# Optimization experiments

Hardware: AMD Instinct MI355X
Metric: run time of the kernel (lower is better)

Reference implementation:

```python
import jax, jax.numpy as jnp
import numpy as np

DIM = 768
HEAD = 12
DK = DIM // HEAD

def setup_inputs() -> dict:
    key = jax.random.key(0)
    ks = jax.random.split(key, 9)
    B, L = 4, 2048
    s = 1.0 / np.sqrt(DIM)
    qkv = jax.random.normal(ks[0], (B, L, DIM), dtype=jnp.float32)
    mask = jnp.ones((B, L), dtype=jnp.int32)
    Wq = jax.random.normal(ks[1], (DIM, DIM), dtype=jnp.float32) * s
    bq = jnp.zeros((DIM,), dtype=jnp.float32)
    Wk = jax.random.normal(ks[2], (DIM, DIM), dtype=jnp.float32) * s
    bk = jnp.zeros((DIM,), dtype=jnp.float32)
    Wv = jax.random.normal(ks[3], (DIM, DIM), dtype=jnp.float32) * s
    bv = jnp.zeros((DIM,), dtype=jnp.float32)
    Wo = jax.random.normal(ks[4], (DIM, DIM), dtype=jnp.float32) * s
    bo = jnp.zeros((DIM,), dtype=jnp.float32)
    return {"qkv": qkv, "mask": mask, "Wq": Wq, "bq": bq, "Wk": Wk, "bk": bk,
            "Wv": Wv, "bv": bv, "Wo": Wo, "bo": bo}

def reference(qkv, mask, Wq, bq, Wk, bk, Wv, bv, Wo, bo):
    B, L, _ = qkv.shape
    def proj(W, b):
        # [B,L,dim] -> [B,H,L,dk]
        return (qkv @ W + b).reshape(B, L, HEAD, DK).transpose(0, 2, 1, 3)
    q, k, v = proj(Wq, bq), proj(Wk, bk), proj(Wv, bv)
    scores = jnp.einsum('bhqd,bhkd->bhqk', q, k) / jnp.sqrt(jnp.float32(DK))
    # mask: [B,L] broadcast over heads and query positions (key axis)
    m = mask[:, None, None, :]  # [B,1,1,L]
    scores = jnp.where(m == 0, jnp.float32(-1e9), scores)
    p = jax.nn.softmax(scores, axis=-1)
    x = jnp.einsum('bhqk,bhkd->bhqd', p, v)  # [B,H,L,dk]
    x = x.transpose(0, 2, 1, 3).reshape(B, L, DIM)
    return x @ Wo + bo
```

## Files before the change

### kernel.cpp

```cpp
#include <hip/hip_runtime.h>
#include <hip/hip_bf16.h>
#include <stdint.h>

#define DIM  768
#define NHEAD 12
#define DK   64
#define BATCH 4
#define SEQ  2048
#define ROWS (BATCH*SEQ)
#define SCL  0.1803368801111204f

typedef __bf16 bf16_t;
typedef bf16_t bf16x8 __attribute__((ext_vector_type(8)));
typedef bf16_t bf16x4 __attribute__((ext_vector_type(4)));
typedef float  f32x4  __attribute__((ext_vector_type(4)));
typedef float  f32x16 __attribute__((ext_vector_type(16)));

typedef unsigned int __attribute__((address_space(1)))* as1p;
typedef unsigned int __attribute__((address_space(3)))* as3p;

__device__ __forceinline__ void gload_lds16(const void* g, void* l) {
    __builtin_amdgcn_global_load_lds((as1p)g, (as3p)l, 16, 0, 0);
}
#define MEMFENCE asm volatile("" ::: "memory")

__global__ void cast_bf16_kernel(const float* __restrict__ in, bf16_t* __restrict__ out) {
    int i = blockIdx.x * 256 + threadIdx.x;
    const float4* p = (const float4*)in;
    float4 a = p[(size_t)i*2], b = p[(size_t)i*2+1];
    bf16x8 v;
    v[0]=(bf16_t)a.x; v[1]=(bf16_t)a.y; v[2]=(bf16_t)a.z; v[3]=(bf16_t)a.w;
    v[4]=(bf16_t)b.x; v[5]=(bf16_t)b.y; v[6]=(bf16_t)b.z; v[7]=(bf16_t)b.w;
    *(bf16x8*)(out + (size_t)i*8) = v;
}

__global__ void wtrans_kernel(const float* __restrict__ W0, const float* __restrict__ W1,
                              const float* __restrict__ W2, const float* __restrict__ W3,
                              bf16_t* __restrict__ T0, bf16_t* __restrict__ T1,
                              bf16_t* __restrict__ T2, bf16_t* __restrict__ T3) {
    const float* W = blockIdx.z==0?W0 : blockIdx.z==1?W1 : blockIdx.z==2?W2 : W3;
    bf16_t*      T = blockIdx.z==0?T0 : blockIdx.z==1?T1 : blockIdx.z==2?T2 : T3;
    __shared__ float tile[32][33];
    int tx = threadIdx.x, ty = threadIdx.y;
    int c = blockIdx.x*32 + tx;
    #pragma unroll
    for (int r = 0; r < 32; r += 8)
        tile[ty+r][tx] = W[(size_t)(blockIdx.y*32 + ty + r)*DIM + c];
    __syncthreads();
    int oc = blockIdx.y*32 + tx;
    #pragma unroll
    for (int r = 0; r < 32; r += 8)
        T[(size_t)(blockIdx.x*32 + ty + r)*DIM + oc] = (bf16_t)tile[tx][ty+r];
}

template<int MODE>
__global__ __launch_bounds__(256) void gemm_kernel(
    const bf16_t* __restrict__ A,
    const bf16_t* __restrict__ WTa, const bf16_t* __restrict__ WTb, const bf16_t* __restrict__ WTc,
    const float* __restrict__ ba, const float* __restrict__ bb, const float* __restrict__ bc,
    bf16_t* __restrict__ Qo, bf16_t* __restrict__ Ko, bf16_t* __restrict__ Vo,
    float* __restrict__ Oo) {
    __shared__ __align__(16) bf16_t As[2][128*32];
    __shared__ __align__(16) bf16_t Bs[2][128*32];
    const int tid = threadIdx.x, wave = tid>>6, lane = tid&63;
    const int wm = wave>>1, wn = wave&1;
    const int b = blockIdx.x;
    const int xcd = b & 7, ib = b >> 3;
    int z, ntile, mtile;
    if (MODE == 0) { z = ib % 3; ntile = (ib/3) % 6; mtile = xcd*8 + ib/18; }
    else           { z = 0;      ntile = ib % 6;     mtile = xcd*8 + ib/6;  }
    const int m0 = mtile*128, n0 = ntile*128;
    const bf16_t* WT  = (z==0) ? WTa : (z==1 ? WTb : WTc);
    const float* bias = (z==0) ? ba  : (z==1 ? bb  : bc);

    f32x4 acc[4][4];
    const f32x4 zf = {0.f,0.f,0.f,0.f};
    #pragma unroll
    for (int m = 0; m < 4; ++m)
        #pragma unroll
        for (int n = 0; n < 4; ++n) acc[m][n] = zf;

    const int srow = wave*32 + (lane>>2);
    const int scol = (lane&3)*8;
    const bf16_t* Ag = A  + (size_t)(m0+srow)*DIM + scol;
    const bf16_t* Bg = WT + (size_t)(n0+srow)*DIM + scol;

    #pragma unroll
    for (int i2 = 0; i2 < 2; ++i2) {
        gload_lds16(Ag + (size_t)(i2*16)*DIM, &As[0][(wave*32 + i2*16)*32]);
        gload_lds16(Bg + (size_t)(i2*16)*DIM, &Bs[0][(wave*32 + i2*16)*32]);
    }

    int cur = 0;
    for (int t = 0; t < DIM/32; ++t) {
        if (t < DIM/32 - 1) {
            const size_t k1 = (size_t)(t+1)*32;
            #pragma unroll
            for (int i2 = 0; i2 < 2; ++i2) {
                gload_lds16(Ag + (size_t)(i2*16)*DIM + k1, &As[cur^1][(wave*32 + i2*16)*32]);
                gload_lds16(Bg + (size_t)(i2*16)*DIM + k1, &Bs[cur^1][(wave*32 + i2*16)*32]);
            }
            asm volatile("s_waitcnt vmcnt(4)" ::: "memory");
        } else {
            asm volatile("s_waitcnt vmcnt(0)" ::: "memory");
        }
        MEMFENCE; __builtin_amdgcn_s_barrier(); MEMFENCE;

        bf16x8 af[4], bfr[4];
        #pragma unroll
        for (int m = 0; m < 4; ++m)
            af[m]  = *(const bf16x8*)&As[cur][(wm*64 + m*16 + (lane&15))*32 + (lane>>4)*8];
        #pragma unroll
        for (int n = 0; n < 4; ++n)
            bfr[n] = *(const bf16x8*)&Bs[cur][(wn*64 + n*16 + (lane&15))*32 + (lane>>4)*8];
        #pragma unroll
        for (int m = 0; m < 4; ++m)
            #pragma unroll
            for (int n = 0; n < 4; ++n)
                acc[m][n] = __builtin_amdgcn_mfma_f32_16x16x32_bf16(af[m], bfr[n], acc[m][n], 0, 0, 0);

        MEMFENCE; __builtin_amdgcn_s_barrier(); MEMFENCE;
        cur ^= 1;
    }

    float bvv[4];
    #pragma unroll
    for (int n = 0; n < 4; ++n) bvv[n] = bias[n0 + wn*64 + n*16 + (lane&15)];

    #pragma unroll
    for (int m = 0; m < 4; ++m) {
        #pragma unroll
        for (int n = 0; n < 4; ++n) {
            #pragma unroll
            for (int r = 0; r < 4; ++r) {
                float val = acc[m][n][r] + bvv[n];
                int R = m0 + wm*64 + m*16 + (lane>>4)*4 + r;
                int C = n0 + wn*64 + n*16 + (lane&15);
                if (MODE == 1) {
                    Oo[(size_t)R*DIM + C] = val;
                } else {
                    int bi = R>>11, li = R&2047, h = C>>6, d = C&63;
                    size_t bh = (size_t)(bi*NHEAD + h);
                    if      (z==0) Qo[(bh*SEQ + li)*DK + d] = (bf16_t)(val*SCL);
                    else if (z==1) Ko[(bh*SEQ + li)*DK + d] = (bf16_t)val;
                    else {
                        int li2 = (li & ~12) | ((li&4)<<1) | ((li&8)>>1);
                        Vo[(bh*DK + d)*SEQ + li2] = (bf16_t)val;
                    }
                }
            }
        }
    }
}

#define NT (SEQ/64)

__global__ __launch_bounds__(256) void attn_kernel(
    const bf16_t* __restrict__ Q, const bf16_t* __restrict__ K, const bf16_t* __restrict__ VT,
    const int* __restrict__ mask, bf16_t* __restrict__ X) {
    __shared__ __align__(16) bf16_t lds[2*8192];
    const int tid = threadIdx.x, wv = tid>>6, lane = tid&63;
    const int lo5 = lane&31, hi5 = lane>>5;
    const int b = blockIdx.x;
    const int xcd = b & 7, ii = b >> 3;
    const int bh = xcd*6 + (ii>>4), qt = ii & 15;
    const int bi = bh/NHEAD, h = bh%NHEAD;
    const bf16_t* Qb = Q  + (size_t)bh*SEQ*DK;
    const bf16_t* Kb = K  + (size_t)bh*SEQ*DK;
    const bf16_t* Vb = VT + (size_t)bh*DK*SEQ;
    const int* mk = mask + (size_t)bi*SEQ + lo5;
    const int q0 = qt*128 + wv*32;

    int mOk = 1;
    {
        const int4* m4 = (const int4*)(mask + (size_t)bi*SEQ);
        #pragma unroll
        for (int i2 = 0; i2 < 8; ++i2) {
            int4 v = m4[lane + i2*64];
            mOk &= (v.x != 0) & (v.y != 0) & (v.z != 0) & (v.w != 0);
        }
    }
    const int mAll = __all(mOk);

    bf16x8 qf[4];
    #pragma unroll
    for (int ks = 0; ks < 4; ++ks)
        qf[ks] = *(const bf16x8*)&Qb[(size_t)(q0 + lo5)*DK + ks*16 + hi5*8];

    f32x16 O0, O1;
    #pragma unroll
    for (int r = 0; r < 16; ++r) { O0[r] = 0.f; O1[r] = 0.f; }
    float lsum = 0.f;

    bf16x8 onesb = {};
    if (hi5 == 0) onesb[0] = (bf16_t)1.0f;

    const int srow  = wv*16 + (lane>>3);
    const int sslot = (lane&7) ^ (srow&7);
    const bf16_t* Kg = Kb + (size_t)srow*DK  + sslot*8;
    const bf16_t* Vg = Vb + (size_t)srow*SEQ + sslot*8;
    int koff[4];
    #pragma unroll
    for (int ks = 0; ks < 4; ++ks) koff[ks] = (((2*ks + hi5) ^ (lo5 & 7)) << 3);

    #pragma unroll
    for (int i = 0; i < 2; ++i) {
        gload_lds16(Kg + (size_t)(i*8)*DK,  lds +        (wv*16 + i*8)*64);
        gload_lds16(Vg + (size_t)(i*8)*SEQ, lds + 4096 + (wv*16 + i*8)*64);
    }

    int cur = 0;
    for (int t = 0; t < NT; ++t) {
        const int kv0 = t*64;
        if (t < NT-1) {
            bf16_t* nb = lds + (cur^1)*8192;
            #pragma unroll
            for (int i = 0; i < 2; ++i) {
                gload_lds16(Kg + (size_t)(kv0+64)*DK + (size_t)(i*8)*DK,  nb +        (wv*16 + i*8)*64);
                gload_lds16(Vg + (kv0+64)            + (size_t)(i*8)*SEQ, nb + 4096 + (wv*16 + i*8)*64);
            }
            asm volatile("s_waitcnt vmcnt(4)" ::: "memory");
        } else {
            asm volatile("s_waitcnt vmcnt(0)" ::: "memory");
        }
        MEMFENCE; __builtin_amdgcn_s_barrier(); MEMFENCE;

        const bf16_t* Kt = lds + cur*8192;
        const bf16_t* Vt = lds + cur*8192 + 4096;

        f32x16 s0, s1;
        #pragma unroll
        for (int r = 0; r < 16; ++r) { s0[r] = -12.f; s1[r] = -12.f; }
        #pragma unroll
        for (int ks = 0; ks < 4; ++ks) {
            bf16x8 a0 = *(const bf16x8*)&Kt[ lo5     *64 + koff[ks]];
            bf16x8 a1 = *(const bf16x8*)&Kt[(32+lo5)*64 + koff[ks]];
            s0 = __builtin_amdgcn_mfma_f32_32x32x16_bf16(a0, qf[ks], s0, 0, 0, 0);
            s1 = __builtin_amdgcn_mfma_f32_32x32x16_bf16(a1, qf[ks], s1, 0, 0, 0);
        }
        if (!mAll) {
            int mv0 = mk[kv0], mv1 = mk[kv0 + 32];
            bf16x8 ba = {};
            ba[0] = mv0 ? (bf16_t)0.f : (bf16_t)(-1024.0f);
            s0 = __builtin_amdgcn_mfma_f32_32x32x16_bf16(ba, onesb, s0, 0, 0, 0);
            ba[0] = mv1 ? (bf16_t)0.f : (bf16_t)(-1024.0f);
            s1 = __builtin_amdgcn_mfma_f32_32x32x16_bf16(ba, onesb, s1, 0, 0, 0);
        }

        #pragma unroll
        for (int r = 0; r < 16; ++r) {
            s0[r] = __builtin_amdgcn_exp2f(s0[r]);
            s1[r] = __builtin_amdgcn_exp2f(s1[r]);
        }
        float t01[16];
        #pragma unroll
        for (int r = 0; r < 16; ++r) t01[r] = s0[r] + s1[r];
        float u[8];
        #pragma unroll
        for (int r = 0; r < 8; ++r) u[r] = t01[r] + t01[r+8];
        float w0 = (u[0]+u[1]) + (u[2]+u[3]);
        float w1 = (u[4]+u[5]) + (u[6]+u[7]);
        float ps = w0 + w1;
        lsum += ps + __shfl_xor(ps, 32);

        bf16x8 pf0, pf1, pf2, pf3;
        #pragma unroll
        for (int j = 0; j < 8; ++j) {
            pf0[j] = (bf16_t)s0[j];
            pf1[j] = (bf16_t)s0[8+j];
            pf2[j] = (bf16_t)s1[j];
            pf3[j] = (bf16_t)s1[8+j];
        }

        #pragma unroll
        for (int ks = 0; ks < 4; ++ks) {
            bf16x8 pb = (ks==0) ? pf0 : (ks==1) ? pf1 : (ks==2) ? pf2 : pf3;
            bf16x8 a0 = *(const bf16x8*)&Vt[ lo5     *64 + koff[ks]];
            bf16x8 a1 = *(const bf16x8*)&Vt[(32+lo5)*64 + koff[ks]];
            O0 = __builtin_amdgcn_mfma_f32_32x32x16_bf16(a0, pb, O0, 0, 0, 0);
            O1 = __builtin_amdgcn_mfma_f32_32x32x16_bf16(a1, pb, O1, 0, 0, 0);
        }
        MEMFENCE; __builtin_amdgcn_s_barrier(); MEMFENCE;
        cur ^= 1;
    }

    float rl = __builtin_amdgcn_rcpf(lsum);
    const size_t rowb = (size_t)(bi*SEQ + q0 + lo5)*DIM + h*DK;
    #pragma unroll
    for (int g = 0; g < 4; ++g) {
        bf16x4 v0, v1;
        #pragma unroll
        for (int j = 0; j < 4; ++j) {
            v0[j] = (bf16_t)(O0[g*4+j] * rl);
            v1[j] = (bf16_t)(O1[g*4+j] * rl);
        }
        *(bf16x4*)&X[rowb + g*8 + hi5*4]      = v0;
        *(bf16x4*)&X[rowb + 32 + g*8 + hi5*4] = v1;
    }
}

extern "C" void kernel_launch(void* const* d_in, const int* in_sizes, int n_in,
                              void* d_out, int out_size, void* d_ws, size_t ws_size,
                              hipStream_t stream) {
    (void)in_sizes; (void)n_in; (void)out_size; (void)ws_size;
    const float* qkv = (const float*)d_in[0];
    const int*  mask = (const int*)d_in[1];
    const float* Wq = (const float*)d_in[2];
    const float* bq = (const float*)d_in[3];
    const float* Wk = (const float*)d_in[4];
    const float* bk = (const float*)d_in[5];
    const float* Wv = (const float*)d_in[6];
    const float* bv = (const float*)d_in[7];
    const float* Wo = (const float*)d_in[8];
    const float* bo = (const float*)d_in[9];
    float* out = (float*)d_out;

    char* ws = (char*)d_ws;
    size_t off = 0;
    auto carve = [&](size_t bytes) { void* p = ws + off; off += (bytes + 255) & ~(size_t)255; return p; };
    const size_t actN = (size_t)ROWS*DIM;
    bf16_t* Abf = (bf16_t*)carve(actN*2);
    bf16_t* WTq = (bf16_t*)carve((size_t)DIM*DIM*2);
    bf16_t* WTk = (bf16_t*)carve((size_t)DIM*DIM*2);
    bf16_t* WTv = (bf16_t*)carve((size_t)DIM*DIM*2);
    bf16_t* WTo = (bf16_t*)carve((size_t)DIM*DIM*2);
    bf16_t* Qb  = (bf16_t*)carve(actN*2);
    bf16_t* Kb  = (bf16_t*)carve(actN*2);
    bf16_t* VTb = (bf16_t*)carve(actN*2);
    bf16_t* Xb  = (bf16_t*)carve(actN*2);

    cast_bf16_kernel<<<dim3(ROWS*DIM/8/256), dim3(256), 0, stream>>>(qkv, Abf);
    wtrans_kernel<<<dim3(24,24,4), dim3(32,8), 0, stream>>>(Wq, Wk, Wv, Wo, WTq, WTk, WTv, WTo);
    gemm_kernel<0><<<dim3(1152), dim3(256), 0, stream>>>(Abf, WTq, WTk, WTv, bq, bk, bv,
                                                         Qb, Kb, VTb, nullptr);
    attn_kernel<<<dim3(768), dim3(256), 0, stream>>>(Qb, Kb, VTb, mask, Xb);
    gemm_kernel<1><<<dim3(384), dim3(256), 0, stream>>>(Xb, WTo, WTo, WTo, bo, bo, bo,
                                                        nullptr, nullptr, nullptr, out);
}
```

Before: 173.2 us.

## Enlarge GEMM tiles to 256x128 with 8 waves and triple-buffered LDS pipeline

The projection GEMMs now use 512-thread blocks, each computing a 256x128 output tile with 8 waves arranged 4x2, which halves the grid size. Global-to-LDS loads switch from double to triple buffering with a two-stage prefetch distance, and the vmcnt waits are adjusted to match. The aim is to hide more memory latency and reuse each B tile across more rows. In exchange, LDS use per block grows to about 72KB and there are fewer blocks (192 for the output projection, below the CU count), which may hurt occupancy and load balance.

```diff
diff --git a/kernel.cpp b/kernel.cpp
--- a/kernel.cpp
+++ b/kernel.cpp
@@ -54,22 +54,22 @@
 }
 
 template<int MODE>
-__global__ __launch_bounds__(256) void gemm_kernel(
+__global__ __launch_bounds__(512) void gemm_kernel(
     const bf16_t* __restrict__ A,
     const bf16_t* __restrict__ WTa, const bf16_t* __restrict__ WTb, const bf16_t* __restrict__ WTc,
     const float* __restrict__ ba, const float* __restrict__ bb, const float* __restrict__ bc,
     bf16_t* __restrict__ Qo, bf16_t* __restrict__ Ko, bf16_t* __restrict__ Vo,
     float* __restrict__ Oo) {
-    __shared__ __align__(16) bf16_t As[2][128*32];
-    __shared__ __align__(16) bf16_t Bs[2][128*32];
+    __shared__ __align__(16) bf16_t As[3][256*32];
+    __shared__ __align__(16) bf16_t Bs[3][128*32];
     const int tid = threadIdx.x, wave = tid>>6, lane = tid&63;
     const int wm = wave>>1, wn = wave&1;
     const int b = blockIdx.x;
     const int xcd = b & 7, ib = b >> 3;
     int z, ntile, mtile;
-    if (MODE == 0) { z = ib % 3; ntile = (ib/3) % 6; mtile = xcd*8 + ib/18; }
-    else           { z = 0;      ntile = ib % 6;     mtile = xcd*8 + ib/6;  }
-    const int m0 = mtile*128, n0 = ntile*128;
+    if (MODE == 0) { z = ib % 3; ntile = (ib/3) % 6; mtile = xcd*4 + ib/18; }
+    else           { z = 0;      ntile = ib % 6;     mtile = xcd*4 + ib/6;  }
+    const int m0 = mtile*256, n0 = ntile*128;
     const bf16_t* WT  = (z==0) ? WTa : (z==1 ? WTb : WTc);
     const float* bias = (z==0) ? ba  : (z==1 ? bb  : bc);
 
@@ -80,27 +80,30 @@
         #pragma unroll
         for (int n = 0; n < 4; ++n) acc[m][n] = zf;
 
-    const int srow = wave*32 + (lane>>2);
+    const int srow = wave*16 + (lane>>2);
     const int scol = (lane&3)*8;
     const bf16_t* Ag = A  + (size_t)(m0+srow)*DIM + scol;
     const bf16_t* Bg = WT + (size_t)(n0+srow)*DIM + scol;
-
-    #pragma unroll
-    for (int i2 = 0; i2 < 2; ++i2) {
-        gload_lds16(Ag + (size_t)(i2*16)*DIM, &As[0][(wave*32 + i2*16)*32]);
-        gload_lds16(Bg + (size_t)(i2*16)*DIM, &Bs[0][(wave*32 + i2*16)*32]);
-    }
-
+    const int aoff0 = (wave*16)*32, aoff1 = (128 + wave*16)*32, boff = (wave*16)*32;
+
+    #define GEMM_STAGE(BUF, KOFF)                                              \
+        gload_lds16(Ag + (KOFF),                     &As[BUF][aoff0]);         \
+        gload_lds16(Ag + (size_t)128*DIM + (KOFF),   &As[BUF][aoff1]);         \
+        gload_lds16(Bg + (KOFF),                     &Bs[BUF][boff]);
+
+    GEMM_STAGE(0, 0)
+    GEMM_STAGE(1, 32)
+
+    const int NTK = DIM/32;
     int cur = 0;
-    for (int t = 0; t < DIM/32; ++t) {
-        if (t < DIM/32 - 1) {
-            const size_t k1 = (size_t)(t+1)*32;
-            #pragma unroll
-            for (int i2 = 0; i2 < 2; ++i2) {
-                gload_lds16(Ag + (size_t)(i2*16)*DIM + k1, &As[cur^1][(wave*32 + i2*16)*32]);
-                gload_lds16(Bg + (size_t)(i2*16)*DIM + k1, &Bs[cur^1][(wave*32 + i2*16)*32]);
-            }
-            asm volatile("s_waitcnt vmcnt(4)" ::: "memory");
+    for (int t = 0; t < NTK; ++t) {
+        if (t + 2 < NTK) {
+            int b2 = cur + 2; if (b2 >= 3) b2 -= 3;
+            const size_t k2 = (size_t)(t+2)*32;
+            GEMM_STAGE(b2, k2)
+            asm volatile("s_waitcnt vmcnt(6)" ::: "memory");
+        } else if (t + 1 < NTK) {
+            asm volatile("s_waitcnt vmcnt(3)" ::: "memory");
         } else {
             asm volatile("s_waitcnt vmcnt(0)" ::: "memory");
         }
@@ -120,8 +123,9 @@
                 acc[m][n] = __builtin_amdgcn_mfma_f32_16x16x32_bf16(af[m], bfr[n], acc[m][n], 0, 0, 0);
 
         MEMFENCE; __builtin_amdgcn_s_barrier(); MEMFENCE;
-        cur ^= 1;
-    }
+        cur = (cur == 2) ? 0 : cur + 1;
+    }
+    #undef GEMM_STAGE
 
     float bvv[4];
     #pragma unroll
@@ -331,9 +335,9 @@
 
     cast_bf16_kernel<<<dim3(ROWS*DIM/8/256), dim3(256), 0, stream>>>(qkv, Abf);
     wtrans_kernel<<<dim3(24,24,4), dim3(32,8), 0, stream>>>(Wq, Wk, Wv, Wo, WTq, WTk, WTv, WTo);
-    gemm_kernel<0><<<dim3(1152), dim3(256), 0, stream>>>(Abf, WTq, WTk, WTv, bq, bk, bv,
-                                                         Qb, Kb, VTb, nullptr);
+    gemm_kernel<0><<<dim3(576), dim3(512), 0, stream>>>(Abf, WTq, WTk, WTv, bq, bk, bv,
+                                                        Qb, Kb, VTb, nullptr);
     attn_kernel<<<dim3(768), dim3(256), 0, stream>>>(Qb, Kb, VTb, mask, Xb);
-    gemm_kernel<1><<<dim3(384), dim3(256), 0, stream>>>(Xb, WTo, WTo, WTo, bo, bo, bo,
+    gemm_kernel<1><<<dim3(192), dim3(512), 0, stream>>>(Xb, WTo, WTo, WTo, bo, bo, bo,
                                                         nullptr, nullptr, nullptr, out);
 }
```

After: 185.3 us. 7.0% more time.

## Use 256x256 tiles with 32x32x16 MFMA and swizzled LDS for QKV projection

Applied to the files above, without the earlier changes.

Splits the projection GEMM into a dedicated QKV kernel with 512 threads, 256x256 output tiles, K-step 64, XOR-swizzled LDS layout and 32x32x16 MFMA instructions, launched as 288 blocks instead of 1152. Larger tiles raise arithmetic intensity and cut redundant global loads, and the swizzle targets LDS bank conflicts. The output projection keeps the old 128x128 tiling in its own simplified kernel. In exchange the bigger tiles use much more LDS and registers per block, and 288 blocks may not fill all CUs well.

```diff
diff --git a/kernel.cpp b/kernel.cpp
--- a/kernel.cpp
+++ b/kernel.cpp
@@ -53,25 +53,117 @@
         T[(size_t)(blockIdx.x*32 + ty + r)*DIM + oc] = (bf16_t)tile[tx][ty+r];
 }
 
-template<int MODE>
-__global__ __launch_bounds__(256) void gemm_kernel(
+__global__ __launch_bounds__(512) void gemm0_kernel(
     const bf16_t* __restrict__ A,
-    const bf16_t* __restrict__ WTa, const bf16_t* __restrict__ WTb, const bf16_t* __restrict__ WTc,
-    const float* __restrict__ ba, const float* __restrict__ bb, const float* __restrict__ bc,
-    bf16_t* __restrict__ Qo, bf16_t* __restrict__ Ko, bf16_t* __restrict__ Vo,
-    float* __restrict__ Oo) {
+    const bf16_t* __restrict__ WTq, const bf16_t* __restrict__ WTk, const bf16_t* __restrict__ WTv,
+    const float* __restrict__ bq, const float* __restrict__ bk, const float* __restrict__ bv,
+    bf16_t* __restrict__ Qo, bf16_t* __restrict__ Ko, bf16_t* __restrict__ Vo) {
+    __shared__ __align__(16) bf16_t As[2][256*64];
+    __shared__ __align__(16) bf16_t Bs[2][256*64];
+    const int tid = threadIdx.x, wave = tid>>6, lane = tid&63;
+    const int lo5 = lane&31, hi5 = lane>>5;
+    const int wm = wave>>2, wn = wave&3;
+    const int b = blockIdx.x;
+    const int xcd = b & 7, ib = b >> 3;
+    const int mtile = xcd*4 + ib/9;
+    const int nn = ib % 9, z = nn/3, ntile = nn%3;
+    const int m0 = mtile*256, n0 = ntile*256;
+    const bf16_t* WT  = (z==0) ? WTq : (z==1 ? WTk : WTv);
+    const float* bias = (z==0) ? bq  : (z==1 ? bk  : bv);
+
+    f32x16 acc[4][2];
+    #pragma unroll
+    for (int m = 0; m < 4; ++m)
+        #pragma unroll
+        for (int n = 0; n < 2; ++n)
+            #pragma unroll
+            for (int r = 0; r < 16; ++r) acc[m][n][r] = 0.f;
+
+    const int srow  = wave*32 + (lane>>3);
+    const int sslot = (lane&7) ^ (srow&7);
+    const bf16_t* Ag = A  + (size_t)(m0+srow)*DIM + sslot*8;
+    const bf16_t* Bg = WT + (size_t)(n0+srow)*DIM + sslot*8;
+    int koff[4];
+    #pragma unroll
+    for (int ks = 0; ks < 4; ++ks) koff[ks] = (((2*ks + hi5) ^ (lo5 & 7)) << 3);
+
+    #define G0STAGE(BUF, K0)                                                     \
+        _Pragma("unroll")                                                        \
+        for (int i2 = 0; i2 < 4; ++i2) {                                         \
+            gload_lds16(Ag + (size_t)(i2*8)*DIM + (K0), &As[BUF][(wave*32 + i2*8)*64]); \
+            gload_lds16(Bg + (size_t)(i2*8)*DIM + (K0), &Bs[BUF][(wave*32 + i2*8)*64]); \
+        }
+
+    G0STAGE(0, 0)
+
+    int cur = 0;
+    const int NTK = DIM/64;
+    for (int t = 0; t < NTK; ++t) {
+        if (t < NTK-1) {
+            G0STAGE(cur^1, (size_t)(t+1)*64)
+            asm volatile("s_waitcnt vmcnt(8)" ::: "memory");
+        } else {
+            asm volatile("s_waitcnt vmcnt(0)" ::: "memory");
+        }
+        MEMFENCE; __builtin_amdgcn_s_barrier(); MEMFENCE;
+
+        #pragma unroll
+        for (int ks = 0; ks < 4; ++ks) {
+            bf16x8 af[4], bfr[2];
+            #pragma unroll
+            for (int m = 0; m < 4; ++m)
+                af[m]  = *(const bf16x8*)&As[cur][(wm*128 + m*32 + lo5)*64 + koff[ks]];
+            #pragma unroll
+            for (int n = 0; n < 2; ++n)
+                bfr[n] = *(const bf16x8*)&Bs[cur][(wn*64 + n*32 + lo5)*64 + koff[ks]];
+            #pragma unroll
+            for (int m = 0; m < 4; ++m)
+                #pragma unroll
+                for (int n = 0; n < 2; ++n)
+                    acc[m][n] = __builtin_amdgcn_mfma_f32_32x32x16_bf16(af[m], bfr[n], acc[m][n], 0, 0, 0);
+        }
+        MEMFENCE; __builtin_amdgcn_s_barrier(); MEMFENCE;
+        cur ^= 1;
+    }
+    #undef G0STAGE
+
+    float bv2[2];
+    #pragma unroll
+    for (int n = 0; n < 2; ++n) bv2[n] = bias[n0 + wn*64 + n*32 + lo5];
+
+    #pragma unroll
+    for (int m = 0; m < 4; ++m) {
+        #pragma unroll
+        for (int n = 0; n < 2; ++n) {
+            #pragma unroll
+            for (int r = 0; r < 16; ++r) {
+                float val = acc[m][n][r] + bv2[n];
+                int R = m0 + wm*128 + m*32 + (r&3) + 8*(r>>2) + 4*hi5;
+                int c = n0 + wn*64 + n*32 + lo5;
+                int bi = R>>11, li = R&2047, h = c>>6, d = c&63;
+                size_t bh = (size_t)(bi*NHEAD + h);
+                if      (z==0) Qo[(bh*SEQ + li)*DK + d] = (bf16_t)(val*SCL);
+                else if (z==1) Ko[(bh*SEQ + li)*DK + d] = (bf16_t)val;
+                else {
+                    int li2 = (li & ~12) | ((li&4)<<1) | ((li&8)>>1);
+                    Vo[(bh*DK + d)*SEQ + li2] = (bf16_t)val;
+                }
+            }
+        }
+    }
+}
+
+__global__ __launch_bounds__(256) void gemm1_kernel(
+    const bf16_t* __restrict__ A, const bf16_t* __restrict__ WT,
+    const float* __restrict__ bias, float* __restrict__ Oo) {
     __shared__ __align__(16) bf16_t As[2][128*32];
     __shared__ __align__(16) bf16_t Bs[2][128*32];
     const int tid = threadIdx.x, wave = tid>>6, lane = tid&63;
     const int wm = wave>>1, wn = wave&1;
     const int b = blockIdx.x;
     const int xcd = b & 7, ib = b >> 3;
-    int z, ntile, mtile;
-    if (MODE == 0) { z = ib % 3; ntile = (ib/3) % 6; mtile = xcd*8 + ib/18; }
-    else           { z = 0;      ntile = ib % 6;     mtile = xcd*8 + ib/6;  }
+    const int ntile = ib % 6, mtile = xcd*8 + ib/6;
     const int m0 = mtile*128, n0 = ntile*128;
-    const bf16_t* WT  = (z==0) ? WTa : (z==1 ? WTb : WTc);
-    const float* bias = (z==0) ? ba  : (z==1 ? bb  : bc);
 
     f32x4 acc[4][4];
     const f32x4 zf = {0.f,0.f,0.f,0.f};
@@ -133,21 +225,9 @@
         for (int n = 0; n < 4; ++n) {
             #pragma unroll
             for (int r = 0; r < 4; ++r) {
-                float val = acc[m][n][r] + bvv[n];
                 int R = m0 + wm*64 + m*16 + (lane>>4)*4 + r;
                 int C = n0 + wn*64 + n*16 + (lane&15);
-                if (MODE == 1) {
-                    Oo[(size_t)R*DIM + C] = val;
-                } else {
-                    int bi = R>>11, li = R&2047, h = C>>6, d = C&63;
-                    size_t bh = (size_t)(bi*NHEAD + h);
-                    if      (z==0) Qo[(bh*SEQ + li)*DK + d] = (bf16_t)(val*SCL);
-                    else if (z==1) Ko[(bh*SEQ + li)*DK + d] = (bf16_t)val;
-                    else {
-                        int li2 = (li & ~12) | ((li&4)<<1) | ((li&8)>>1);
-                        Vo[(bh*DK + d)*SEQ + li2] = (bf16_t)val;
-                    }
-                }
+                Oo[(size_t)R*DIM + C] = acc[m][n][r] + bvv[n];
             }
         }
     }
@@ -331,9 +411,8 @@
 
     cast_bf16_kernel<<<dim3(ROWS*DIM/8/256), dim3(256), 0, stream>>>(qkv, Abf);
     wtrans_kernel<<<dim3(24,24,4), dim3(32,8), 0, stream>>>(Wq, Wk, Wv, Wo, WTq, WTk, WTv, WTo);
-    gemm_kernel<0><<<dim3(1152), dim3(256), 0, stream>>>(Abf, WTq, WTk, WTv, bq, bk, bv,
-                                                         Qb, Kb, VTb, nullptr);
+    gemm0_kernel<<<dim3(288), dim3(512), 0, stream>>>(Abf, WTq, WTk, WTv, bq, bk, bv,
+                                                      Qb, Kb, VTb);
     attn_kernel<<<dim3(768), dim3(256), 0, stream>>>(Qb, Kb, VTb, mask, Xb);
-    gemm_kernel<1><<<dim3(384), dim3(256), 0, stream>>>(Xb, WTo, WTo, WTo, bo, bo, bo,
-                                                        nullptr, nullptr, nullptr, out);
-}
+    gemm1_kernel<<<dim3(384), dim3(256), 0, stream>>>(Xb, WTo, bo, out);
+}
```

After: 186.5 us. 7.6% more time.

## Load GEMM fragments directly from global memory, dropping LDS staging and barriers

Applied to the files above, without the earlier changes.

The projection GEMM kernel no longer stages A and W tiles through double-buffered shared memory with async global-to-LDS loads and barriers. Each wave now loads its MFMA operand fragments straight from global memory into registers, relying on the cache for reuse. The block-to-tile mapping for the QKV mode also changes so that consecutive blocks walk the N tiles within one weight matrix. This removes LDS traffic and synchronisation, but adds redundant global loads across waves, strided 16-byte accesses, and no explicit prefetch to hide latency.

```diff
diff --git a/kernel.cpp b/kernel.cpp
--- a/kernel.cpp
+++ b/kernel.cpp
@@ -60,15 +60,14 @@
     const float* __restrict__ ba, const float* __restrict__ bb, const float* __restrict__ bc,
     bf16_t* __restrict__ Qo, bf16_t* __restrict__ Ko, bf16_t* __restrict__ Vo,
     float* __restrict__ Oo) {
-    __shared__ __align__(16) bf16_t As[2][128*32];
-    __shared__ __align__(16) bf16_t Bs[2][128*32];
     const int tid = threadIdx.x, wave = tid>>6, lane = tid&63;
     const int wm = wave>>1, wn = wave&1;
+    const int lo4 = lane&15, hi2 = lane>>4;
     const int b = blockIdx.x;
     const int xcd = b & 7, ib = b >> 3;
     int z, ntile, mtile;
-    if (MODE == 0) { z = ib % 3; ntile = (ib/3) % 6; mtile = xcd*8 + ib/18; }
-    else           { z = 0;      ntile = ib % 6;     mtile = xcd*8 + ib/6;  }
+    if (MODE == 0) { int nz = ib % 18; z = nz/6; ntile = nz%6; mtile = xcd*8 + ib/18; }
+    else           { z = 0;            ntile = ib % 6;         mtile = xcd*8 + ib/6;  }
     const int m0 = mtile*128, n0 = ntile*128;
     const bf16_t* WT  = (z==0) ? WTa : (z==1 ? WTb : WTc);
     const float* bias = (z==0) ? ba  : (z==1 ? bb  : bc);
@@ -80,52 +79,33 @@
         #pragma unroll
         for (int n = 0; n < 4; ++n) acc[m][n] = zf;
 
-    const int srow = wave*32 + (lane>>2);
-    const int scol = (lane&3)*8;
-    const bf16_t* Ag = A  + (size_t)(m0+srow)*DIM + scol;
-    const bf16_t* Bg = WT + (size_t)(n0+srow)*DIM + scol;
-
-    #pragma unroll
-    for (int i2 = 0; i2 < 2; ++i2) {
-        gload_lds16(Ag + (size_t)(i2*16)*DIM, &As[0][(wave*32 + i2*16)*32]);
-        gload_lds16(Bg + (size_t)(i2*16)*DIM, &Bs[0][(wave*32 + i2*16)*32]);
-    }
-
-    int cur = 0;
+    const bf16_t* Ar[4];
+    const bf16_t* Br[4];
+    #pragma unroll
+    for (int m = 0; m < 4; ++m)
+        Ar[m] = A  + (size_t)(m0 + wm*64 + m*16 + lo4)*DIM + hi2*8;
+    #pragma unroll
+    for (int n = 0; n < 4; ++n)
+        Br[n] = WT + (size_t)(n0 + wn*64 + n*16 + lo4)*DIM + hi2*8;
+
+    #pragma unroll 4
     for (int t = 0; t < DIM/32; ++t) {
-        if (t < DIM/32 - 1) {
-            const size_t k1 = (size_t)(t+1)*32;
-            #pragma unroll
-            for (int i2 = 0; i2 < 2; ++i2) {
-                gload_lds16(Ag + (size_t)(i2*16)*DIM + k1, &As[cur^1][(wave*32 + i2*16)*32]);
-                gload_lds16(Bg + (size_t)(i2*16)*DIM + k1, &Bs[cur^1][(wave*32 + i2*16)*32]);
-            }
-            asm volatile("s_waitcnt vmcnt(4)" ::: "memory");
-        } else {
-            asm volatile("s_waitcnt vmcnt(0)" ::: "memory");
-        }
-        MEMFENCE; __builtin_amdgcn_s_barrier(); MEMFENCE;
-
+        const int k0 = t*32;
         bf16x8 af[4], bfr[4];
         #pragma unroll
-        for (int m = 0; m < 4; ++m)
-            af[m]  = *(const bf16x8*)&As[cur][(wm*64 + m*16 + (lane&15))*32 + (lane>>4)*8];
-        #pragma unroll
-        for (int n = 0; n < 4; ++n)
-            bfr[n] = *(const bf16x8*)&Bs[cur][(wn*64 + n*16 + (lane&15))*32 + (lane>>4)*8];
+        for (int m = 0; m < 4; ++m) af[m]  = *(const bf16x8*)(Ar[m] + k0);
+        #pragma unroll
+        for (int n = 0; n < 4; ++n) bfr[n] = *(const bf16x8*)(Br[n] + k0);
         #pragma unroll
         for (int m = 0; m < 4; ++m)
             #pragma unroll
             for (int n = 0; n < 4; ++n)
                 acc[m][n] = __builtin_amdgcn_mfma_f32_16x16x32_bf16(af[m], bfr[n], acc[m][n], 0, 0, 0);
-
-        MEMFENCE; __builtin_amdgcn_s_barrier(); MEMFENCE;
-        cur ^= 1;
     }
 
     float bvv[4];
     #pragma unroll
-    for (int n = 0; n < 4; ++n) bvv[n] = bias[n0 + wn*64 + n*16 + (lane&15)];
+    for (int n = 0; n < 4; ++n) bvv[n] = bias[n0 + wn*64 + n*16 + lo4];
 
     #pragma unroll
     for (int m = 0; m < 4; ++m) {
@@ -134,8 +114,8 @@
             #pragma unroll
             for (int r = 0; r < 4; ++r) {
                 float val = acc[m][n][r] + bvv[n];
-                int R = m0 + wm*64 + m*16 + (lane>>4)*4 + r;
-                int C = n0 + wn*64 + n*16 + (lane&15);
+                int R = m0 + wm*64 + m*16 + hi2*4 + r;
+                int C = n0 + wn*64 + n*16 + lo4;
                 if (MODE == 1) {
                     Oo[(size_t)R*DIM + C] = val;
                 } else {
```

After: 277.6 us. 1.6x slower.
